# Optimization experiments

Hardware: AMD Instinct MI355X
Metric: run time of the kernel (lower is better)

Reference implementation:

```python
import jax, jax.numpy as jnp
import numpy as np

EPS = 1e-5

def bn_relu(y, g, b):
    # BatchNorm1d in training mode: stats over (B, L) per channel, biased variance
    mu = jnp.mean(y, axis=(0, 2), keepdims=True)
    var = jnp.var(y, axis=(0, 2), keepdims=True)
    yn = (y - mu) * jax.lax.rsqrt(var + EPS)
    return jax.nn.relu(yn * g[None, :, None] + b[None, :, None])

def conv1x1_pad1(x, W):
    # Conv1d(k=1, padding=1, bias=False): pointwise matmul then zero-pad length by 1 each side
    y = jnp.einsum('bcl,oc->bol', x, W)
    return jnp.pad(y, ((0, 0), (0, 0), (1, 1)))

def conv1x1(x, W, b):
    return jnp.einsum('bcl,oc->bol', x, W) + b[None, :, None]

def conv3_pad1(x, W):
    # Conv1d(k=3, padding=1, bias=False); W: [O, C, 3]
    return jax.lax.conv_general_dilated(x, W, window_strides=(1,), padding=((1, 1),),
                                        dimension_numbers=('NCH', 'OIH', 'NCH'))

def pam(f, Wq, bq, Wk, bk, Wv, bv, gamma):
    q = conv1x1(f, Wq, bq)          # [B, C//8, L]
    k = conv1x1(f, Wk, bk)          # [B, C//8, L]
    v = conv1x1(f, Wv, bv)          # [B, C, L]
    energy = jnp.einsum('bql,bqm->blm', q, k)   # [B, L, L]
    attn = jax.nn.softmax(energy, axis=-1)
    out = jnp.einsum('bcm,blm->bcl', v, attn)
    return gamma * out + f

def cam(f, gamma):
    energy = jnp.einsum('bcl,bdl->bcd', f, f)    # [B, C, C]
    energy_new = jnp.max(energy, axis=-1, keepdims=True) - energy
    attn = jax.nn.softmax(energy_new, axis=-1)
    out = jnp.einsum('bcd,bdl->bcl', attn, f)
    return gamma * out + f

def setup_inputs() -> dict:
    key = jax.random.key(0)
    ks = jax.random.split(key, 24)
    B, C, L = 8, 256, 2046
    IC, OC = C // 4, 128  # inter_channels=64, out_channels
    s = 0.05
    d = {
        'x':   jax.random.normal(ks[0], (B, C, L), jnp.float32),
        'W5a': jax.random.normal(ks[1], (IC, C), jnp.float32) * s,
        'g5a': jnp.ones((IC,), jnp.float32), 'b5a': jnp.zeros((IC,), jnp.float32),
        'W5c': jax.random.normal(ks[2], (IC, C), jnp.float32) * s,
        'g5c': jnp.ones((IC,), jnp.float32), 'b5c': jnp.zeros((IC,), jnp.float32),
        'Wq':  jax.random.normal(ks[3], (IC // 8, IC), jnp.float32) * s,
        'bq':  jnp.zeros((IC // 8,), jnp.float32),
        'Wk':  jax.random.normal(ks[4], (IC // 8, IC), jnp.float32) * s,
        'bk':  jnp.zeros((IC // 8,), jnp.float32),
        'Wv':  jax.random.normal(ks[5], (IC, IC), jnp.float32) * s,
        'bv':  jnp.zeros((IC,), jnp.float32),
        'gamma_pam': jnp.full((1,), 0.1, jnp.float32),
        'gamma_cam': jnp.full((1,), 0.1, jnp.float32),
        'W51': jax.random.normal(ks[6], (IC, IC, 3), jnp.float32) * s,
        'g51': jnp.ones((IC,), jnp.float32), 'b51': jnp.zeros((IC,), jnp.float32),
        'W52': jax.random.normal(ks[7], (IC, IC, 3), jnp.float32) * s,
        'g52': jnp.ones((IC,), jnp.float32), 'b52': jnp.zeros((IC,), jnp.float32),
        'W6':  jax.random.normal(ks[8], (OC, IC), jnp.float32) * s,
        'b6':  jnp.zeros((OC,), jnp.float32),
        'W7':  jax.random.normal(ks[9], (OC, IC), jnp.float32) * s,
        'b7':  jnp.zeros((OC,), jnp.float32),
        'W8':  jax.random.normal(ks[10], (OC, IC), jnp.float32) * s,
        'b8':  jnp.zeros((OC,), jnp.float32),
    }
    return d

def reference(x, W5a, g5a, b5a, W5c, g5c, b5c, Wq, bq, Wk, bk, Wv, bv,
              gamma_pam, gamma_cam, W51, g51, b51, W52, g52, b52,
              W6, b6, W7, b7, W8, b8):
    # dropout (p=0.1) treated as identity (eval mode)
    feat1 = bn_relu(conv1x1_pad1(x, W5a), g5a, b5a)          # [B, IC, L+2]
    sa_feat = pam(feat1, Wq, bq, Wk, bk, Wv, bv, gamma_pam)
    sa_conv = bn_relu(conv3_pad1(sa_feat, W51), g51, b51)
    sa_output = conv1x1(sa_conv, W6, b6)                     # [B, OC, L+2]
    feat2 = bn_relu(conv1x1_pad1(x, W5c), g5c, b5c)
    sc_feat = cam(feat2, gamma_cam)
    sc_conv = bn_relu(conv3_pad1(sc_feat, W52), g52, b52)
    sc_output = conv1x1(sc_conv, W7, b7)
    feat_sum = sa_conv + sc_conv
    sasc = conv1x1(feat_sum, W8, b8)
    # pool == 'maxpool' selects AdaptiveAvgPool1d(1) in the original (note swap)
    sasc = jnp.mean(sasc, axis=-1)                            # [B, OC]
    return (sasc, sa_output, sc_output)
```

## Files before the change

### kernel.cpp

```cpp
#include <hip/hip_runtime.h>
#include <math.h>

#define B 8
#define C 256
#define L 2046
#define LP 2048
#define IC 64
#define OC 128
#define BN_EPS 1e-5f
#define INVN (1.f / 16384.f)

#define OFF_Y1T    0u
#define OFF_Y2C    524288u
#define OFF_Y51T   2097152u
#define OFF_Y52T   2621440u
#define OFF_VB     3145728u
#define OFF_QT     3670016u
#define OFF_KT     3735552u
#define OFF_EPART  3866624u
#define OFF_STATS1 4423680u
#define OFF_STATS2 4424704u
#define OFF_W5BF   4425728u
#define OFF_W67    4442112u
#define OFF_WT     4450304u
#define OFF_WQKV   4462592u
#define OFF_BQKV   4465152u

typedef __attribute__((ext_vector_type(8))) short bshort8;
typedef __attribute__((ext_vector_type(4))) float f32x4;

__device__ __forceinline__ unsigned short f2bf(float f) {
    union { float f; unsigned int u; } v; v.f = f;
    return (unsigned short)((v.u + 0x8000u) >> 16);
}
__device__ __forceinline__ float bf2f(unsigned short u) {
    union { unsigned int i; float f; } v; v.i = ((unsigned int)u) << 16;
    return v.f;
}
__device__ __forceinline__ unsigned int pk2(float a, float b) {
    union { float f; unsigned int u; } va, vb; va.f = a; vb.f = b;
    return __builtin_amdgcn_perm(vb.u + 0x8000u, va.u + 0x8000u, 0x07060302u);
}

__device__ __forceinline__ void load_coef(const float* __restrict__ STATS,
        const float* __restrict__ g, const float* __restrict__ beta,
        int base, int cnt, float* cA, float* cB) {
    int t = threadIdx.x;
    if (t < cnt) {
        int ch = base + t;
        float s = STATS[ch * 2] + STATS[256 + ch * 2] + STATS[512 + ch * 2] + STATS[768 + ch * 2];
        float q = STATS[ch * 2 + 1] + STATS[256 + ch * 2 + 1] + STATS[512 + ch * 2 + 1] + STATS[768 + ch * 2 + 1];
        float mu = s * INVN;
        float var = q * INVN - mu * mu;
        float A = g[t] * rsqrtf(var + BN_EPS);
        cA[t] = A;
        cB[t] = beta[t] - mu * A;
    }
}

__global__ __launch_bounds__(256) void k_wprep(
        const float* __restrict__ W5a, const float* __restrict__ W5c,
        const float* __restrict__ W6, const float* __restrict__ W7,
        const float* __restrict__ W51, const float* __restrict__ W52,
        const float* __restrict__ Wq, const float* __restrict__ Wk,
        const float* __restrict__ Wv, const float* __restrict__ bq,
        const float* __restrict__ bk, const float* __restrict__ bv,
        const float* __restrict__ b8,
        unsigned short* __restrict__ W5BF, unsigned short* __restrict__ W67,
        unsigned short* __restrict__ WT, unsigned short* __restrict__ WQKV,
        float* __restrict__ BQKV, float* __restrict__ STATS1,
        float* __restrict__ STATS2, float* __restrict__ out_sasc) {
    int i = blockIdx.x * 256 + threadIdx.x;
    if (i < 32768) {
        int o = i >> 8, c = i & 255;
        W5BF[i] = f2bf(o < 64 ? W5a[o * 256 + c] : W5c[(o - 64) * 256 + c]);
    } else if (i < 49152) {
        int j = i - 32768; int g = j >> 13; int r = j & 8191;
        W67[j] = f2bf(g ? W7[r] : W6[r]);
    } else if (i < 73728) {
        int j = i - 49152;
        int c = j & 63, o = (j >> 6) & 63, wt = j >> 12; int w = wt / 3, t = wt % 3;
        const float* Ws = w ? W52 : W51;
        WT[j] = f2bf(Ws[(o * 64 + c) * 3 + t]);
    } else if (i < 78848) {
        int j = i - 73728; int o = j >> 6, c = j & 63;
        float v = o < 8 ? Wq[o * 64 + c] : (o < 16 ? Wk[(o - 8) * 64 + c] : Wv[(o - 16) * 64 + c]);
        WQKV[j] = f2bf(v);
    } else if (i < 78928) {
        int o = i - 78848;
        BQKV[o] = o < 8 ? bq[o] : (o < 16 ? bk[o - 8] : bv[o - 16]);
    } else if (i < 80976) {
        int j = i - 78928;
        if (j < 1024) STATS1[j] = 0.f; else STATS2[j - 1024] = 0.f;
    } else if (i < 82000) {
        int j = i - 80976;
        out_sasc[j] = b8[j & 127];
    }
}

__global__ __launch_bounds__(256) void k_conv1(const float* __restrict__ x,
        const unsigned short* __restrict__ W5BF,
        unsigned short* __restrict__ Y1T, unsigned short* __restrict__ Y2C,
        float* __restrict__ STATS1) {
    __shared__ unsigned short xt[64][264];
    __shared__ float lds_part[4][64];
    int lt = blockIdx.x, b = blockIdx.y;
    int l0 = lt * 64;
    int t = threadIdx.x;
    {
        int j = t & 63, cg = t >> 6;
        int ls = l0 - 1 + j;
        bool ok = (ls >= 0) && (ls < L);
        const float* xs = x + (size_t)(b * C + cg * 64) * L + ls;
        unsigned short* row = &xt[j][cg * 64];
#pragma unroll
        for (int c8 = 0; c8 < 8; ++c8) {
            unsigned int pk[4];
#pragma unroll
            for (int i = 0; i < 4; ++i) {
                float v0 = ok ? xs[(size_t)(c8 * 8 + 2 * i) * L] : 0.f;
                float v1 = ok ? xs[(size_t)(c8 * 8 + 2 * i + 1) * L] : 0.f;
                pk[i] = pk2(v0, v1);
            }
            *(uint4*)(row + c8 * 8) = *(const uint4*)pk;
        }
    }
    __syncthreads();
    int w = t >> 6, lane = t & 63, n = lane & 15, quad = lane >> 4;
    bshort8 wf[2][8];
#pragma unroll
    for (int oi = 0; oi < 2; ++oi)
#pragma unroll
        for (int kt = 0; kt < 8; ++kt)
            wf[oi][kt] = *(const bshort8*)(W5BF + (size_t)((w * 2 + oi) * 16 + n) * C + kt * 32 + quad * 8);
    f32x4 acc[2][4];
#pragma unroll
    for (int oi = 0; oi < 2; ++oi)
#pragma unroll
        for (int sub = 0; sub < 4; ++sub) acc[oi][sub] = (f32x4){0.f, 0.f, 0.f, 0.f};
#pragma unroll
    for (int sub = 0; sub < 4; ++sub) {
        int lloc = sub * 16 + n;
#pragma unroll
        for (int kt = 0; kt < 8; ++kt) {
            bshort8 xb = *(const bshort8*)(&xt[lloc][kt * 32 + quad * 8]);
            acc[0][sub] = __builtin_amdgcn_mfma_f32_16x16x32_bf16(wf[0][kt], xb, acc[0][sub], 0, 0, 0);
            acc[1][sub] = __builtin_amdgcn_mfma_f32_16x16x32_bf16(wf[1][kt], xb, acc[1][sub], 0, 0, 0);
        }
    }
    if (w < 2) {
#pragma unroll
        for (int sub = 0; sub < 4; ++sub) {
            int lp = l0 + sub * 16 + n;
#pragma unroll
            for (int oi = 0; oi < 2; ++oi) {
                int ot = w * 2 + oi;
                uint2 pv;
                pv.x = pk2(acc[oi][sub][0], acc[oi][sub][1]);
                pv.y = pk2(acc[oi][sub][2], acc[oi][sub][3]);
                *(uint2*)(Y1T + ((size_t)(b * LP + lp)) * IC + ot * 16 + quad * 4) = pv;
            }
        }
    } else {
#pragma unroll
        for (int oi = 0; oi < 2; ++oi) {
            int ot = (w - 2) * 2 + oi;
#pragma unroll
            for (int r = 0; r < 4; ++r) {
                int o = ot * 16 + quad * 4 + r;
                unsigned short* dst = Y2C + ((size_t)(b * IC + o)) * LP + l0;
#pragma unroll
                for (int sub = 0; sub < 4; ++sub)
                    dst[sub * 16 + n] = f2bf(acc[oi][sub][r]);
            }
        }
    }
#pragma unroll
    for (int oi = 0; oi < 2; ++oi)
#pragma unroll
        for (int r = 0; r < 4; ++r) {
            float s = 0.f, q = 0.f;
#pragma unroll
            for (int sub = 0; sub < 4; ++sub) {
                float v = acc[oi][sub][r];
                s += v; q += v * v;
            }
#pragma unroll
            for (int msk = 1; msk < 16; msk <<= 1) {
                s += __shfl_xor(s, msk, 64);
                q += __shfl_xor(q, msk, 64);
            }
            if (n == 0) {
                int ci = oi * 16 + quad * 4 + r;
                lds_part[w][ci * 2] = s;
                lds_part[w][ci * 2 + 1] = q;
            }
        }
    __syncthreads();
    {
        int ch = t >> 1, wsrc = ch >> 5;
        int idx = ((ch & 31) << 1) | (t & 1);
        atomicAdd(&STATS1[(blockIdx.x & 3) * 256 + t], lds_part[wsrc][idx]);
    }
}

__device__ void role_qkv(char* dynsm, int lt, int b,
        const unsigned short* __restrict__ Y1T, const float* __restrict__ STATS1,
        const float* __restrict__ g5a, const float* __restrict__ b5a,
        const unsigned short* __restrict__ WQKV, const float* __restrict__ BQKV,
        unsigned short* __restrict__ QT, unsigned short* __restrict__ KT,
        unsigned short* __restrict__ VB) {
    float* cA = (float*)dynsm;
    float* cB = cA + 64;
    load_coef(STATS1, g5a, b5a, 0, 64, cA, cB);
    __syncthreads();
    int t = threadIdx.x;
    int w = t >> 6, lane = t & 63, n = lane & 15, quad = lane >> 4;
    int lrow = lt * 64 + w * 16 + n;
    bshort8 fb[2];
#pragma unroll
    for (int kt = 0; kt < 2; ++kt) {
        bshort8 raw = *(const bshort8*)(Y1T + ((size_t)(b * LP + lrow)) * IC + kt * 32 + quad * 8);
        bshort8 f;
#pragma unroll
        for (int j = 0; j < 8; ++j) {
            int c = kt * 32 + quad * 8 + j;
            float v = fmaxf(fmaf(cA[c], bf2f((unsigned short)raw[j]), cB[c]), 0.f);
            ((unsigned short*)&f)[j] = f2bf(v);
        }
        fb[kt] = f;
    }
    f32x4 acc[5];
#pragma unroll
    for (int ot = 0; ot < 5; ++ot) {
        f32x4 a = {0.f, 0.f, 0.f, 0.f};
#pragma unroll
        for (int kt = 0; kt < 2; ++kt) {
            bshort8 wf = *(const bshort8*)(WQKV + (size_t)(ot * 16 + n) * IC + kt * 32 + quad * 8);
            a = __builtin_amdgcn_mfma_f32_16x16x32_bf16(wf, fb[kt], a, 0, 0, 0);
        }
        acc[ot] = a;
    }
#pragma unroll
    for (int ot = 0; ot < 5; ++ot)
#pragma unroll
        for (int r = 0; r < 4; ++r) {
            int o = ot * 16 + quad * 4 + r;
            unsigned short bv16 = f2bf(acc[ot][r] + BQKV[o]);
            if (ot == 0) {
                if (o < 8) QT[((size_t)(b * LP + lrow)) * 8 + o] = bv16;
                else KT[((size_t)(b * LP + lrow)) * 8 + (o - 8)] = bv16;
            } else {
                VB[((size_t)(b * IC + (o - 16))) * LP + lrow] = bv16;
            }
        }
}

__device__ void role_gram(char* dynsm, int blk, int b,
        const unsigned short* __restrict__ Y2C, const float* __restrict__ STATS1,
        const float* __restrict__ g5c, const float* __restrict__ b5c,
        float* __restrict__ EPART) {
    float* cA = (float*)dynsm;
    float* cB = cA + 64;
    load_coef(STATS1, g5c, b5c, 64, 64, cA, cB);
    __syncthreads();
    int t = threadIdx.x;
    int w = t >> 6, lane = t & 63, n = lane & 15, quad = lane >> 4;
    f32x4 acc[4][4];
#pragma unroll
    for (int ti = 0; ti < 4; ++ti)
#pragma unroll
        for (int tj = 0; tj < 4; ++tj) acc[ti][tj] = (f32x4){0.f, 0.f, 0.f, 0.f};
    for (int chunk = 0; chunk < 4; ++chunk) {
        int lb = (blk * 4 + w) * 128 + chunk * 32 + quad * 8;
        bshort8 frag[4];
#pragma unroll
        for (int g = 0; g < 4; ++g) {
            int c = g * 16 + n;
            bshort8 raw = *(const bshort8*)(Y2C + ((size_t)(b * IC + c)) * LP + lb);
            bshort8 f;
            float A = cA[c], Bc = cB[c];
#pragma unroll
            for (int j = 0; j < 8; ++j)
                ((unsigned short*)&f)[j] = f2bf(fmaxf(fmaf(A, bf2f((unsigned short)raw[j]), Bc), 0.f));
            frag[g] = f;
        }
#pragma unroll
        for (int ti = 0; ti < 4; ++ti)
#pragma unroll
            for (int tj = 0; tj < 4; ++tj)
                acc[ti][tj] = __builtin_amdgcn_mfma_f32_16x16x32_bf16(frag[ti], frag[tj], acc[ti][tj], 0, 0, 0);
    }
    float* ep = EPART + ((size_t)(b * 16 + blk * 4 + w)) * 4096;
#pragma unroll
    for (int ti = 0; ti < 4; ++ti)
#pragma unroll
        for (int tj = 0; tj < 4; ++tj)
#pragma unroll
            for (int r = 0; r < 4; ++r)
                ep[(ti * 16 + quad * 4 + r) * 64 + tj * 16 + n] = acc[ti][tj][r];
}

__global__ __launch_bounds__(256) void k_fuse1(
        const unsigned short* __restrict__ Y1T, const unsigned short* __restrict__ Y2C,
        const float* __restrict__ STATS1,
        const float* __restrict__ g5a, const float* __restrict__ b5a,
        const float* __restrict__ g5c, const float* __restrict__ b5c,
        const unsigned short* __restrict__ WQKV, const float* __restrict__ BQKV,
        unsigned short* __restrict__ QT, unsigned short* __restrict__ KT,
        unsigned short* __restrict__ VB, float* __restrict__ EPART) {
    extern __shared__ char dynsm[];
    int idx = blockIdx.x;
    if (idx < 256) role_qkv(dynsm, idx & 31, idx >> 5, Y1T, STATS1, g5a, b5a,
                            WQKV, BQKV, QT, KT, VB);
    else { int g = idx - 256; role_gram(dynsm, g & 3, g >> 2, Y2C, STATS1, g5c, b5c, EPART); }
}

__device__ __forceinline__ void conv3_from_tile(const unsigned short* tile,
        const unsigned short* __restrict__ WT, unsigned short* __restrict__ dst,
        int b, int l0, float* lds_part, float* __restrict__ STATS2,
        int og, int blockx) {
    int t = threadIdx.x;
    int w = t >> 6, lane = t & 63, n = lane & 15, quad = lane >> 4;
    int lrow = l0 + w * 16 + n;
    f32x4 acc[4];
#pragma unroll
    for (int ot = 0; ot < 4; ++ot) acc[ot] = (f32x4){0.f, 0.f, 0.f, 0.f};
#pragma unroll
    for (int t3 = 0; t3 < 3; ++t3) {
        int trow = w * 16 + n + t3;
        bshort8 fb0 = *(const bshort8*)(tile + trow * 72 + quad * 8);
        bshort8 fb1 = *(const bshort8*)(tile + trow * 72 + 32 + quad * 8);
#pragma unroll
        for (int ot = 0; ot < 4; ++ot) {
            bshort8 w0 = *(const bshort8*)(WT + ((size_t)(t3 * 64 + ot * 16 + n)) * IC + quad * 8);
            bshort8 w1 = *(const bshort8*)(WT + ((size_t)(t3 * 64 + ot * 16 + n)) * IC + 32 + quad * 8);
            acc[ot] = __builtin_amdgcn_mfma_f32_16x16x32_bf16(w0, fb0, acc[ot], 0, 0, 0);
            acc[ot] = __builtin_amdgcn_mfma_f32_16x16x32_bf16(w1, fb1, acc[ot], 0, 0, 0);
        }
    }
#pragma unroll
    for (int ot = 0; ot < 4; ++ot) {
        uint2 pv;
        pv.x = pk2(acc[ot][0], acc[ot][1]);
        pv.y = pk2(acc[ot][2], acc[ot][3]);
        *(uint2*)(dst + ((size_t)(b * LP + lrow)) * IC + ot * 16 + quad * 4) = pv;
    }
#pragma unroll
    for (int ot = 0; ot < 4; ++ot)
#pragma unroll
        for (int r = 0; r < 4; ++r) {
            float s = acc[ot][r], q = s * s;
#pragma unroll
            for (int msk = 1; msk < 16; msk <<= 1) {
                s += __shfl_xor(s, msk, 64);
                q += __shfl_xor(q, msk, 64);
            }
            if (n == 0) {
                int cch = ot * 16 + quad * 4 + r;
                lds_part[w * 128 + cch * 2] = s;
                lds_part[w * 128 + cch * 2 + 1] = q;
            }
        }
    __syncthreads();
    if (t < 128) {
        float s = lds_part[t] + lds_part[128 + t] + lds_part[256 + t] + lds_part[384 + t];
        atomicAdd(&STATS2[(blockx & 3) * 256 + og * 128 + t], s);
    }
}

__device__ void role_pam_full(char* dynsm, int qt, int b,
        const unsigned short* __restrict__ qT, const unsigned short* __restrict__ kT,
        const unsigned short* __restrict__ vb,
        const unsigned short* __restrict__ Y1T, const float* __restrict__ STATS1,
        const float* __restrict__ g5a, const float* __restrict__ b5a,
        const float* __restrict__ gamma, const unsigned short* __restrict__ WT,
        unsigned short* __restrict__ Y51T, float* __restrict__ STATS2) {
    unsigned short* vs0 = (unsigned short*)dynsm;
    unsigned short* vs1 = vs0 + 4608;
    unsigned short* ps  = vs1 + 4608;
    float* os = (float*)dynsm;
    unsigned short* tile = ps;
    float* cA = (float*)(dynsm + 27648);
    float* cB = cA + 64;
    float* dn = cB + 64;
    float* lds_part = dn + 64;
    int base = qt * 62 - 1;
    int tid = threadIdx.x;
    int wq = tid >> 6, lane = tid & 63, n = lane & 15, quad = lane >> 4;
    int srow = tid >> 2, schn = tid & 3;
    load_coef(STATS1, g5a, b5a, 0, 64, cA, cB);
    int qrow = base + wq * 16 + n;
    int qcl = qrow < 0 ? 0 : (qrow > LP - 1 ? LP - 1 : qrow);
    bshort8 qa = {};
    if (quad == 0)
        qa = *(const bshort8*)(qT + ((size_t)(b * LP + qcl)) * 8);
    f32x4 acc[4];
#pragma unroll
    for (int s = 0; s < 4; ++s) acc[s] = (f32x4){0.f, 0.f, 0.f, 0.f};
    float li[4] = {0.f, 0.f, 0.f, 0.f};
    unsigned short* pw = ps + wq * 16 * 72;

    {
        const unsigned short* src = vb + ((size_t)(b * IC + srow)) * LP + schn * 16;
        unsigned short* d = vs0 + srow * 72 + schn * 16;
        *(bshort8*)d = *(const bshort8*)src;
        *(bshort8*)(d + 8) = *(const bshort8*)(src + 8);
    }
    bshort8 kb[4];
#pragma unroll
    for (int s = 0; s < 4; ++s) kb[s] = (bshort8){};
    if (quad == 0) {
#pragma unroll
        for (int s = 0; s < 4; ++s)
            kb[s] = *(const bshort8*)(kT + ((size_t)(b * LP + s * 16 + n)) * 8);
    }
    __syncthreads();
    for (int it = 0; it < 32; ++it) {
        unsigned short* cur = (it & 1) ? vs1 : vs0;
        unsigned short* nxt = (it & 1) ? vs0 : vs1;
        if (it < 31) {
            const unsigned short* src = vb + ((size_t)(b * IC + srow)) * LP + (it + 1) * 64 + schn * 16;
            unsigned short* d = nxt + srow * 72 + schn * 16;
            *(bshort8*)d = *(const bshort8*)src;
            *(bshort8*)(d + 8) = *(const bshort8*)(src + 8);
        }
        bshort8 kn[4];
#pragma unroll
        for (int s = 0; s < 4; ++s) kn[s] = (bshort8){};
        if (it < 31 && quad == 0) {
            int m1 = (it + 1) * 64;
#pragma unroll
            for (int s = 0; s < 4; ++s)
                kn[s] = *(const bshort8*)(kT + ((size_t)(b * LP + m1 + s * 16 + n)) * 8);
        }
        f32x4 sc[4];
#pragma unroll
        for (int s = 0; s < 4; ++s)
            sc[s] = __builtin_amdgcn_mfma_f32_16x16x32_bf16(qa, kb[s],
                        (f32x4){0.f, 0.f, 0.f, 0.f}, 0, 0, 0);
#pragma unroll
        for (int s = 0; s < 4; ++s)
#pragma unroll
            for (int r = 0; r < 4; ++r) {
                float p = __expf(sc[s][r]);
                li[r] += p;
                pw[(quad * 4 + r) * 72 + s * 16 + n] = f2bf(p);
            }
#pragma unroll
        for (int step = 0; step < 2; ++step) {
            bshort8 pa = *(const bshort8*)(pw + n * 72 + step * 32 + quad * 8);
#pragma unroll
            for (int s = 0; s < 4; ++s) {
                bshort8 vf = *(const bshort8*)(cur + (s * 16 + n) * 72 + step * 32 + quad * 8);
                acc[s] = __builtin_amdgcn_mfma_f32_16x16x32_bf16(pa, vf, acc[s], 0, 0, 0);
            }
        }
        __syncthreads();
#pragma unroll
        for (int s = 0; s < 4; ++s) kb[s] = kn[s];
    }
#pragma unroll
    for (int s = 0; s < 4; ++s)
#pragma unroll
        for (int r = 0; r < 4; ++r)
            os[(s * 16 + n) * 65 + wq * 16 + quad * 4 + r] = acc[s][r];
#pragma unroll
    for (int r = 0; r < 4; ++r) {
        float s_ = li[r];
#pragma unroll
        for (int msk = 1; msk < 16; msk <<= 1) s_ += __shfl_xor(s_, msk, 64);
        if (n == 0) dn[wq * 16 + quad * 4 + r] = s_;
    }
    __syncthreads();
    float gm = gamma[0];
    {
        int c = tid >> 2, qc = tid & 3;
#pragma unroll
        for (int i = 0; i < 16; ++i) {
            int r = qc * 16 + i;
            int absr = base + r;
            float val = 0.f;
            if (absr >= 0 && absr < LP) {
                unsigned short raw = Y1T[((size_t)(b * LP + absr)) * IC + c];
                float f1v = fmaxf(fmaf(cA[c], bf2f(raw), cB[c]), 0.f);
                val = fmaf(gm, os[c * 65 + r] / dn[r], f1v);
            }
            tile[r * 72 + c] = f2bf(val);
        }
    }
    __syncthreads();
    {
        int j = wq * 16 + n;
        int absout = base + 1 + j;
        bool valid = (j < 62) && (absout < LP);
        f32x4 a3[4];
#pragma unroll
        for (int ot = 0; ot < 4; ++ot) a3[ot] = (f32x4){0.f, 0.f, 0.f, 0.f};
#pragma unroll
        for (int t3 = 0; t3 < 3; ++t3) {
            bshort8 fb0 = *(const bshort8*)(tile + (j + t3) * 72 + quad * 8);
            bshort8 fb1 = *(const bshort8*)(tile + (j + t3) * 72 + 32 + quad * 8);
#pragma unroll
            for (int ot = 0; ot < 4; ++ot) {
                bshort8 w0 = *(const bshort8*)(WT + ((size_t)(t3 * 64 + ot * 16 + n)) * IC + quad * 8);
                bshort8 w1 = *(const bshort8*)(WT + ((size_t)(t3 * 64 + ot * 16 + n)) * IC + 32 + quad * 8);
                a3[ot] = __builtin_amdgcn_mfma_f32_16x16x32_bf16(w0, fb0, a3[ot], 0, 0, 0);
                a3[ot] = __builtin_amdgcn_mfma_f32_16x16x32_bf16(w1, fb1, a3[ot], 0, 0, 0);
            }
        }
        if (valid) {
#pragma unroll
            for (int ot = 0; ot < 4; ++ot) {
                uint2 pv;
                pv.x = pk2(a3[ot][0], a3[ot][1]);
                pv.y = pk2(a3[ot][2], a3[ot][3]);
                *(uint2*)(Y51T + ((size_t)(b * LP + absout)) * IC + ot * 16 + quad * 4) = pv;
            }
        }
#pragma unroll
        for (int ot = 0; ot < 4; ++ot)
#pragma unroll
            for (int r = 0; r < 4; ++r) {
                float s = valid ? a3[ot][r] : 0.f;
                float q = s * s;
#pragma unroll
                for (int msk = 1; msk < 16; msk <<= 1) {
                    s += __shfl_xor(s, msk, 64);
                    q += __shfl_xor(q, msk, 64);
                }
                if (n == 0) {
                    int cch = ot * 16 + quad * 4 + r;
                    lds_part[wq * 128 + cch * 2] = s;
                    lds_part[wq * 128 + cch * 2 + 1] = q;
                }
            }
        __syncthreads();
        if (tid < 128) {
            float s = lds_part[tid] + lds_part[128 + tid] + lds_part[256 + tid] + lds_part[384 + tid];
            atomicAdd(&STATS2[(qt & 3) * 256 + tid], s);
        }
    }
}

__device__ void role_cam_full(char* dynsm, int lt, int b,
        const float* __restrict__ EPART, const unsigned short* __restrict__ Y2C,
        const float* __restrict__ STATS1,
        const float* __restrict__ g5c, const float* __restrict__ b5c,
        const float* __restrict__ gamma, const unsigned short* __restrict__ WT,
        unsigned short* __restrict__ Y52T, float* __restrict__ STATS2) {
    float* as = (float*)dynsm;
    float* cA = as + 4096; float* cB = cA + 64;
    unsigned short* tile = (unsigned short*)(cB + 64);
    float* lds_part = (float*)(tile + 4752);
    int l0 = lt * 64;
    int t = threadIdx.x;
    load_coef(STATS1, g5c, b5c, 64, 64, cA, cB);
    for (int idx = t; idx < 4096; idx += 256) {
        float s = 0.f;
#pragma unroll
        for (int ch = 0; ch < 16; ++ch) s += EPART[((size_t)(b * 16 + ch)) * 4096 + idx];
        as[idx] = s;
    }
    __syncthreads();
    {
        int row = t >> 2, qd = t & 3;
        float v[16];
#pragma unroll
        for (int i = 0; i < 16; ++i) v[i] = as[row * 64 + qd * 16 + i];
        float mn = v[0];
#pragma unroll
        for (int i = 1; i < 16; ++i) mn = fminf(mn, v[i]);
        mn = fminf(mn, __shfl_xor(mn, 1, 64));
        mn = fminf(mn, __shfl_xor(mn, 2, 64));
        float s = 0.f;
#pragma unroll
        for (int i = 0; i < 16; ++i) { v[i] = __expf(mn - v[i]); s += v[i]; }
        s += __shfl_xor(s, 1, 64);
        s += __shfl_xor(s, 2, 64);
        float inv = 1.f / s;
#pragma unroll
        for (int i = 0; i < 16; ++i) as[row * 64 + qd * 16 + i] = v[i] * inv;
    }
    __syncthreads();
    float gm = gamma[0];
    {
        int lq = t & 63, cg = t >> 6;
        const unsigned short* fb = Y2C + (size_t)b * IC * LP + l0 + lq;
        float acc[16];
#pragma unroll
        for (int i = 0; i < 16; ++i) acc[i] = 0.f;
        for (int d4 = 0; d4 < 16; ++d4) {
            float fv[4];
#pragma unroll
            for (int i = 0; i < 4; ++i) {
                int d = 4 * d4 + i;
                fv[i] = fmaxf(fmaf(cA[d], bf2f(fb[(size_t)d * LP]), cB[d]), 0.f);
            }
#pragma unroll
            for (int cc = 0; cc < 16; ++cc) {
                const float4 a4 = *reinterpret_cast<const float4*>(as + (cg * 16 + cc) * 64 + d4 * 4);
                acc[cc] += a4.x * fv[0] + a4.y * fv[1] + a4.z * fv[2] + a4.w * fv[3];
            }
        }
#pragma unroll
        for (int cc = 0; cc < 16; ++cc) {
            int c = cg * 16 + cc;
            float res = fmaxf(fmaf(cA[c], bf2f(fb[(size_t)c * LP]), cB[c]), 0.f);
            tile[(1 + lq) * 72 + c] = f2bf(fmaf(gm, acc[cc], res));
        }
    }
    float* fcol = lds_part;
    if (t < 128) {
        int row = t >> 6;
        int ch = t & 63;
        int l = l0 - 1 + row * 65;
        float v = 0.f;
        if (l >= 0 && l < LP)
            v = fmaxf(fmaf(cA[ch], bf2f(Y2C[(size_t)b * IC * LP + (size_t)ch * LP + l]), cB[ch]), 0.f);
        fcol[row * 64 + ch] = v;
    }
    __syncthreads();
    if (t < 128) {
        int sel = t & 1;
        int row = sel ? 65 : 0;
        int ch = t >> 1;
        int l = l0 - 1 + (sel ? 65 : 0);
        float val = 0.f;
        if (l >= 0 && l < LP) {
            const float* fc = fcol + sel * 64;
            float a = 0.f;
#pragma unroll 8
            for (int d = 0; d < 64; ++d) a = fmaf(as[ch * 64 + d], fc[d], a);
            val = fmaf(gm, a, fc[ch]);
        }
        tile[row * 72 + ch] = f2bf(val);
    }
    __syncthreads();
    conv3_from_tile(tile, WT, Y52T, b, l0, lds_part, STATS2, 1, lt);
}

__global__ __launch_bounds__(256) void k_fuse2(
        const unsigned short* __restrict__ QT, const unsigned short* __restrict__ KT,
        const unsigned short* __restrict__ VB,
        const unsigned short* __restrict__ Y1T, const unsigned short* __restrict__ Y2C,
        const float* __restrict__ STATS1,
        const float* __restrict__ g5a, const float* __restrict__ b5a,
        const float* __restrict__ g5c, const float* __restrict__ b5c,
        const float* __restrict__ gpam, const float* __restrict__ gcam,
        const float* __restrict__ EPART, const unsigned short* __restrict__ WTall,
        unsigned short* __restrict__ Y51T, unsigned short* __restrict__ Y52T,
        float* __restrict__ STATS2) {
    extern __shared__ char dynsm[];
    int idx = blockIdx.x;
    if (idx < 272) {
        int b = idx / 34; int qt = idx - b * 34;
        role_pam_full(dynsm, qt, b, QT, KT, VB, Y1T, STATS1, g5a, b5a, gpam,
                      WTall, Y51T, STATS2);
    } else {
        int g = idx - 272;
        role_cam_full(dynsm, g & 31, g >> 5, EPART, Y2C, STATS1, g5c, b5c, gcam,
                      WTall + 12288, Y52T, STATS2);
    }
}

__global__ __launch_bounds__(256) void k_final(const unsigned short* __restrict__ Y51T,
        const unsigned short* __restrict__ Y52T, const float* __restrict__ STATS2,
        const float* __restrict__ g51, const float* __restrict__ b51,
        const float* __restrict__ g52, const float* __restrict__ b52,
        const unsigned short* __restrict__ W67,
        const float* __restrict__ b6, const float* __restrict__ b7,
        const float* __restrict__ W8,
        float* __restrict__ out_sa, float* __restrict__ out_sc,
        float* __restrict__ out_sasc) {
    __shared__ float cA[128], cB[128];
    __shared__ float fsw[4][64];
    __shared__ float chsum[64];
    int lt = blockIdx.x, og = blockIdx.y, b = blockIdx.z;
    int t = threadIdx.x;
    if (t < 128) {
        float s = STATS2[t * 2] + STATS2[256 + t * 2] + STATS2[512 + t * 2] + STATS2[768 + t * 2];
        float q = STATS2[t * 2 + 1] + STATS2[256 + t * 2 + 1] + STATS2[512 + t * 2 + 1] + STATS2[768 + t * 2 + 1];
        float mu = s * INVN, var = q * INVN - mu * mu;
        float gv = t < 64 ? g51[t] : g52[t - 64];
        float bv = t < 64 ? b51[t] : b52[t - 64];
        float A = gv * rsqrtf(var + BN_EPS);
        cA[t] = A; cB[t] = bv - mu * A;
    }
    __syncthreads();
    int w = t >> 6, lane = t & 63, n = lane & 15, quad = lane >> 4;
    int lrow = lt * 64 + w * 16 + n;
    float fs_lane[16];
    bshort8 ba[2], bb[2];
#pragma unroll
    for (int kt = 0; kt < 2; ++kt) {
        bshort8 ra = *(const bshort8*)(Y51T + ((size_t)(b * LP + lrow)) * IC + kt * 32 + quad * 8);
        bshort8 rb = *(const bshort8*)(Y52T + ((size_t)(b * LP + lrow)) * IC + kt * 32 + quad * 8);
        bshort8 fa, fb;
#pragma unroll
        for (int j = 0; j < 8; ++j) {
            int c = kt * 32 + quad * 8 + j;
            float v1 = fmaxf(fmaf(cA[c], bf2f((unsigned short)ra[j]), cB[c]), 0.f);
            float v2 = fmaxf(fmaf(cA[64 + c], bf2f((unsigned short)rb[j]), cB[64 + c]), 0.f);
            ((unsigned short*)&fa)[j] = f2bf(v1);
            ((unsigned short*)&fb)[j] = f2bf(v2);
            fs_lane[kt * 8 + j] = v1 + v2;
        }
        ba[kt] = fa; bb[kt] = fb;
    }
    f32x4 accA[4], accB[4];
#pragma unroll
    for (int ot = 0; ot < 4; ++ot) {
        accA[ot] = (f32x4){0.f, 0.f, 0.f, 0.f};
        accB[ot] = (f32x4){0.f, 0.f, 0.f, 0.f};
    }
#pragma unroll
    for (int ot = 0; ot < 4; ++ot)
#pragma unroll
        for (int kt = 0; kt < 2; ++kt) {
            bshort8 wa = *(const bshort8*)(W67 + (size_t)(og * 64 + ot * 16 + n) * IC + kt * 32 + quad * 8);
            bshort8 wb = *(const bshort8*)(W67 + 8192 + (size_t)(og * 64 + ot * 16 + n) * IC + kt * 32 + quad * 8);
            accA[ot] = __builtin_amdgcn_mfma_f32_16x16x32_bf16(wa, ba[kt], accA[ot], 0, 0, 0);
            accB[ot] = __builtin_amdgcn_mfma_f32_16x16x32_bf16(wb, bb[kt], accB[ot], 0, 0, 0);
        }
#pragma unroll
    for (int ot = 0; ot < 4; ++ot)
#pragma unroll
        for (int r = 0; r < 4; ++r) {
            int o = og * 64 + ot * 16 + quad * 4 + r;
            out_sa[((size_t)(b * OC + o)) * LP + lrow] = accA[ot][r] + b6[o];
            out_sc[((size_t)(b * OC + o)) * LP + lrow] = accB[ot][r] + b7[o];
        }
    if (og == 0) {
#pragma unroll
        for (int i = 0; i < 16; ++i) {
            float s = fs_lane[i];
#pragma unroll
            for (int msk = 1; msk < 16; msk <<= 1) s += __shfl_xor(s, msk, 64);
            if (n == 0) {
                int c = (i >> 3) * 32 + quad * 8 + (i & 7);
                fsw[w][c] = s;
            }
        }
        __syncthreads();
        if (t < 64) chsum[t] = fsw[0][t] + fsw[1][t] + fsw[2][t] + fsw[3][t];
        __syncthreads();
        if (t < 128) {
            float s = 0.f;
            for (int c = 0; c < 64; ++c) s = fmaf(W8[t * 64 + c], chsum[c], s);
            atomicAdd(&out_sasc[b * OC + t], s * (1.f / (float)LP));
        }
    }
}

extern "C" void kernel_launch(void* const* d_in, const int* in_sizes, int n_in,
                              void* d_out, int out_size, void* d_ws, size_t ws_size,
                              hipStream_t stream) {
    (void)in_sizes; (void)n_in; (void)out_size; (void)ws_size;
    const float* x    = (const float*)d_in[0];
    const float* W5a  = (const float*)d_in[1];
    const float* g5a  = (const float*)d_in[2];
    const float* b5a  = (const float*)d_in[3];
    const float* W5c  = (const float*)d_in[4];
    const float* g5c  = (const float*)d_in[5];
    const float* b5c  = (const float*)d_in[6];
    const float* Wq   = (const float*)d_in[7];
    const float* bq   = (const float*)d_in[8];
    const float* Wk   = (const float*)d_in[9];
    const float* bk   = (const float*)d_in[10];
    const float* Wv   = (const float*)d_in[11];
    const float* bv   = (const float*)d_in[12];
    const float* gpam = (const float*)d_in[13];
    const float* gcam = (const float*)d_in[14];
    const float* W51  = (const float*)d_in[15];
    const float* g51  = (const float*)d_in[16];
    const float* b51  = (const float*)d_in[17];
    const float* W52  = (const float*)d_in[18];
    const float* g52  = (const float*)d_in[19];
    const float* b52  = (const float*)d_in[20];
    const float* W6   = (const float*)d_in[21];
    const float* b6   = (const float*)d_in[22];
    const float* W7   = (const float*)d_in[23];
    const float* b7   = (const float*)d_in[24];
    const float* W8   = (const float*)d_in[25];
    const float* b8   = (const float*)d_in[26];

    float* ws = (float*)d_ws;
    float* out = (float*)d_out;
    unsigned short* Y1T  = (unsigned short*)(ws + OFF_Y1T);
    unsigned short* Y2C  = (unsigned short*)(ws + OFF_Y2C);
    unsigned short* Y51T = (unsigned short*)(ws + OFF_Y51T);
    unsigned short* Y52T = (unsigned short*)(ws + OFF_Y52T);
    unsigned short* VB   = (unsigned short*)(ws + OFF_VB);
    unsigned short* QT   = (unsigned short*)(ws + OFF_QT);
    unsigned short* KT   = (unsigned short*)(ws + OFF_KT);
    float* EPART  = ws + OFF_EPART;
    float* STATS1 = ws + OFF_STATS1;
    float* STATS2 = ws + OFF_STATS2;
    unsigned short* W5BF = (unsigned short*)(ws + OFF_W5BF);
    unsigned short* W67  = (unsigned short*)(ws + OFF_W67);
    unsigned short* WT   = (unsigned short*)(ws + OFF_WT);
    unsigned short* WQKV = (unsigned short*)(ws + OFF_WQKV);
    float* BQKV = ws + OFF_BQKV;

    float* out_sa = out + B * OC;
    float* out_sc = out + B * OC + (size_t)B * OC * LP;

    k_wprep<<<321, 256, 0, stream>>>(W5a, W5c, W6, W7, W51, W52, Wq, Wk, Wv,
                                     bq, bk, bv, b8, W5BF, W67, WT, WQKV, BQKV,
                                     STATS1, STATS2, out);
    k_conv1<<<dim3(32, B), 256, 0, stream>>>(x, W5BF, Y1T, Y2C, STATS1);
    k_fuse1<<<288, 256, 512, stream>>>(Y1T, Y2C, STATS1, g5a, b5a, g5c, b5c,
                                       WQKV, BQKV, QT, KT, VB, EPART);
    k_fuse2<<<528, 256, 30464, stream>>>(QT, KT, VB, Y1T, Y2C, STATS1,
                                         g5a, b5a, g5c, b5c, gpam, gcam,
                                         EPART, WT, Y51T, Y52T, STATS2);
    k_final<<<dim3(32, 2, B), 256, 0, stream>>>(Y51T, Y52T, STATS2, g51, b51, g52, b52,
                                                W67, b6, b7, W8, out_sa, out_sc, out);
}
```

Baseline: 220.5 us.

## Double V staging chunk to 128 columns in PAM loop, halving barriers

```diff
diff --git a/kernel.cpp b/kernel.cpp
--- a/kernel.cpp
+++ b/kernel.cpp
@@ -44,8 +44,7 @@
 
 __device__ __forceinline__ void load_coef(const float* __restrict__ STATS,
         const float* __restrict__ g, const float* __restrict__ beta,
-        int base, int cnt, float* cA, float* cB) {
-    int t = threadIdx.x;
+        int base, int cnt, float* cA, float* cB, int t) {
     if (t < cnt) {
         int ch = base + t;
         float s = STATS[ch * 2] + STATS[256 + ch * 2] + STATS[512 + ch * 2] + STATS[768 + ch * 2];
@@ -212,7 +211,7 @@
         unsigned short* __restrict__ VB) {
     float* cA = (float*)dynsm;
     float* cB = cA + 64;
-    load_coef(STATS1, g5a, b5a, 0, 64, cA, cB);
+    load_coef(STATS1, g5a, b5a, 0, 64, cA, cB, threadIdx.x);
     __syncthreads();
     int t = threadIdx.x;
     int w = t >> 6, lane = t & 63, n = lane & 15, quad = lane >> 4;
@@ -262,7 +261,7 @@
         float* __restrict__ EPART) {
     float* cA = (float*)dynsm;
     float* cB = cA + 64;
-    load_coef(STATS1, g5c, b5c, 64, 64, cA, cB);
+    load_coef(STATS1, g5c, b5c, 64, 64, cA, cB, threadIdx.x);
     __syncthreads();
     int t = threadIdx.x;
     int w = t >> 6, lane = t & 63, n = lane & 15, quad = lane >> 4;
@@ -316,59 +315,6 @@
     else { int g = idx - 256; role_gram(dynsm, g & 3, g >> 2, Y2C, STATS1, g5c, b5c, EPART); }
 }
 
-__device__ __forceinline__ void conv3_from_tile(const unsigned short* tile,
-        const unsigned short* __restrict__ WT, unsigned short* __restrict__ dst,
-        int b, int l0, float* lds_part, float* __restrict__ STATS2,
-        int og, int blockx) {
-    int t = threadIdx.x;
-    int w = t >> 6, lane = t & 63, n = lane & 15, quad = lane >> 4;
-    int lrow = l0 + w * 16 + n;
-    f32x4 acc[4];
-#pragma unroll
-    for (int ot = 0; ot < 4; ++ot) acc[ot] = (f32x4){0.f, 0.f, 0.f, 0.f};
-#pragma unroll
-    for (int t3 = 0; t3 < 3; ++t3) {
-        int trow = w * 16 + n + t3;
-        bshort8 fb0 = *(const bshort8*)(tile + trow * 72 + quad * 8);
-        bshort8 fb1 = *(const bshort8*)(tile + trow * 72 + 32 + quad * 8);
-#pragma unroll
-        for (int ot = 0; ot < 4; ++ot) {
-            bshort8 w0 = *(const bshort8*)(WT + ((size_t)(t3 * 64 + ot * 16 + n)) * IC + quad * 8);
-            bshort8 w1 = *(const bshort8*)(WT + ((size_t)(t3 * 64 + ot * 16 + n)) * IC + 32 + quad * 8);
-            acc[ot] = __builtin_amdgcn_mfma_f32_16x16x32_bf16(w0, fb0, acc[ot], 0, 0, 0);
-            acc[ot] = __builtin_amdgcn_mfma_f32_16x16x32_bf16(w1, fb1, acc[ot], 0, 0, 0);
-        }
-    }
-#pragma unroll
-    for (int ot = 0; ot < 4; ++ot) {
-        uint2 pv;
-        pv.x = pk2(acc[ot][0], acc[ot][1]);
-        pv.y = pk2(acc[ot][2], acc[ot][3]);
-        *(uint2*)(dst + ((size_t)(b * LP + lrow)) * IC + ot * 16 + quad * 4) = pv;
-    }
-#pragma unroll
-    for (int ot = 0; ot < 4; ++ot)
-#pragma unroll
-        for (int r = 0; r < 4; ++r) {
-            float s = acc[ot][r], q = s * s;
-#pragma unroll
-            for (int msk = 1; msk < 16; msk <<= 1) {
-                s += __shfl_xor(s, msk, 64);
-                q += __shfl_xor(q, msk, 64);
-            }
-            if (n == 0) {
-                int cch = ot * 16 + quad * 4 + r;
-                lds_part[w * 128 + cch * 2] = s;
-                lds_part[w * 128 + cch * 2 + 1] = q;
-            }
-        }
-    __syncthreads();
-    if (t < 128) {
-        float s = lds_part[t] + lds_part[128 + t] + lds_part[256 + t] + lds_part[384 + t];
-        atomicAdd(&STATS2[(blockx & 3) * 256 + og * 128 + t], s);
-    }
-}
-
 __device__ void role_pam_full(char* dynsm, int qt, int b,
         const unsigned short* __restrict__ qT, const unsigned short* __restrict__ kT,
         const unsigned short* __restrict__ vb,
@@ -377,19 +323,19 @@
         const float* __restrict__ gamma, const unsigned short* __restrict__ WT,
         unsigned short* __restrict__ Y51T, float* __restrict__ STATS2) {
     unsigned short* vs0 = (unsigned short*)dynsm;
-    unsigned short* vs1 = vs0 + 4608;
-    unsigned short* ps  = vs1 + 4608;
+    unsigned short* vs1 = vs0 + 8704;
+    unsigned short* ps  = (unsigned short*)(dynsm + 34816);
+    unsigned short* tile = ps;
     float* os = (float*)dynsm;
-    unsigned short* tile = ps;
-    float* cA = (float*)(dynsm + 27648);
+    float* cA = (float*)(dynsm + 44032);
     float* cB = cA + 64;
     float* dn = cB + 64;
     float* lds_part = dn + 64;
     int base = qt * 62 - 1;
     int tid = threadIdx.x;
     int wq = tid >> 6, lane = tid & 63, n = lane & 15, quad = lane >> 4;
-    int srow = tid >> 2, schn = tid & 3;
-    load_coef(STATS1, g5a, b5a, 0, 64, cA, cB);
+    int sch = tid >> 2, skf = (tid & 3) * 32;
+    load_coef(STATS1, g5a, b5a, 0, 64, cA, cB, tid);
     int qrow = base + wq * 16 + n;
     int qcl = qrow < 0 ? 0 : (qrow > LP - 1 ? LP - 1 : qrow);
     bshort8 qa = {};
@@ -400,12 +346,15 @@
     for (int s = 0; s < 4; ++s) acc[s] = (f32x4){0.f, 0.f, 0.f, 0.f};
     float li[4] = {0.f, 0.f, 0.f, 0.f};
     unsigned short* pw = ps + wq * 16 * 72;
+    const unsigned short* vsrc = vb + ((size_t)(b * IC + sch)) * LP + skf;
 
     {
-        const unsigned short* src = vb + ((size_t)(b * IC + srow)) * LP + schn * 16;
-        unsigned short* d = vs0 + srow * 72 + schn * 16;
-        *(bshort8*)d = *(const bshort8*)src;
-        *(bshort8*)(d + 8) = *(const bshort8*)(src + 8);
+        bshort8 v0[4];
+#pragma unroll
+        for (int i = 0; i < 4; ++i) v0[i] = *(const bshort8*)(vsrc + i * 8);
+        unsigned short* d = vs0 + sch * 136 + skf;
+#pragma unroll
+        for (int i = 0; i < 4; ++i) *(bshort8*)(d + i * 8) = v0[i];
     }
     bshort8 kb[4];
 #pragma unroll
@@ -416,49 +365,58 @@
             kb[s] = *(const bshort8*)(kT + ((size_t)(b * LP + s * 16 + n)) * 8);
     }
     __syncthreads();
-    for (int it = 0; it < 32; ++it) {
-        unsigned short* cur = (it & 1) ? vs1 : vs0;
-        unsigned short* nxt = (it & 1) ? vs0 : vs1;
-        if (it < 31) {
-            const unsigned short* src = vb + ((size_t)(b * IC + srow)) * LP + (it + 1) * 64 + schn * 16;
-            unsigned short* d = nxt + srow * 72 + schn * 16;
-            *(bshort8*)d = *(const bshort8*)src;
-            *(bshort8*)(d + 8) = *(const bshort8*)(src + 8);
-        }
-        bshort8 kn[4];
-#pragma unroll
-        for (int s = 0; s < 4; ++s) kn[s] = (bshort8){};
-        if (it < 31 && quad == 0) {
-            int m1 = (it + 1) * 64;
+    for (int sup = 0; sup < 16; ++sup) {
+        unsigned short* cur = (sup & 1) ? vs1 : vs0;
+        unsigned short* nxt = (sup & 1) ? vs0 : vs1;
+        bshort8 vrg[4];
+        if (sup < 15) {
+#pragma unroll
+            for (int i = 0; i < 4; ++i)
+                vrg[i] = *(const bshort8*)(vsrc + (sup + 1) * 128 + i * 8);
+        }
+        __builtin_amdgcn_sched_barrier(0);
+#pragma unroll
+        for (int ki = 0; ki < 2; ++ki) {
+            int g = sup * 2 + ki;
+            bshort8 kn[4];
+#pragma unroll
+            for (int s = 0; s < 4; ++s) kn[s] = (bshort8){};
+            if (g < 31 && quad == 0) {
+#pragma unroll
+                for (int s = 0; s < 4; ++s)
+                    kn[s] = *(const bshort8*)(kT + ((size_t)(b * LP + (g + 1) * 64 + s * 16 + n)) * 8);
+            }
+            f32x4 sc[4];
 #pragma unroll
             for (int s = 0; s < 4; ++s)
-                kn[s] = *(const bshort8*)(kT + ((size_t)(b * LP + m1 + s * 16 + n)) * 8);
-        }
-        f32x4 sc[4];
-#pragma unroll
-        for (int s = 0; s < 4; ++s)
-            sc[s] = __builtin_amdgcn_mfma_f32_16x16x32_bf16(qa, kb[s],
-                        (f32x4){0.f, 0.f, 0.f, 0.f}, 0, 0, 0);
-#pragma unroll
-        for (int s = 0; s < 4; ++s)
-#pragma unroll
-            for (int r = 0; r < 4; ++r) {
-                float p = __expf(sc[s][r]);
-                li[r] += p;
-                pw[(quad * 4 + r) * 72 + s * 16 + n] = f2bf(p);
-            }
-#pragma unroll
-        for (int step = 0; step < 2; ++step) {
-            bshort8 pa = *(const bshort8*)(pw + n * 72 + step * 32 + quad * 8);
-#pragma unroll
-            for (int s = 0; s < 4; ++s) {
-                bshort8 vf = *(const bshort8*)(cur + (s * 16 + n) * 72 + step * 32 + quad * 8);
-                acc[s] = __builtin_amdgcn_mfma_f32_16x16x32_bf16(pa, vf, acc[s], 0, 0, 0);
-            }
+                sc[s] = __builtin_amdgcn_mfma_f32_16x16x32_bf16(qa, kb[s],
+                            (f32x4){0.f, 0.f, 0.f, 0.f}, 0, 0, 0);
+#pragma unroll
+            for (int s = 0; s < 4; ++s)
+#pragma unroll
+                for (int r = 0; r < 4; ++r) {
+                    float p = __expf(sc[s][r]);
+                    li[r] += p;
+                    pw[(quad * 4 + r) * 72 + s * 16 + n] = f2bf(p);
+                }
+#pragma unroll
+            for (int step = 0; step < 2; ++step) {
+                bshort8 pa = *(const bshort8*)(pw + n * 72 + step * 32 + quad * 8);
+#pragma unroll
+                for (int s = 0; s < 4; ++s) {
+                    bshort8 vf = *(const bshort8*)(cur + (s * 16 + n) * 136 + ki * 64 + step * 32 + quad * 8);
+                    acc[s] = __builtin_amdgcn_mfma_f32_16x16x32_bf16(pa, vf, acc[s], 0, 0, 0);
+                }
+            }
+#pragma unroll
+            for (int s = 0; s < 4; ++s) kb[s] = kn[s];
+        }
+        if (sup < 15) {
+            unsigned short* d = nxt + sch * 136 + skf;
+#pragma unroll
+            for (int i = 0; i < 4; ++i) *(bshort8*)(d + i * 8) = vrg[i];
         }
         __syncthreads();
-#pragma unroll
-        for (int s = 0; s < 4; ++s) kb[s] = kn[s];
     }
 #pragma unroll
     for (int s = 0; s < 4; ++s)
@@ -543,20 +501,71 @@
     }
 }
 
-__device__ void role_cam_full(char* dynsm, int lt, int b,
+__device__ __forceinline__ void conv3_from_tile_cam(const unsigned short* tile,
+        const unsigned short* __restrict__ WT, unsigned short* __restrict__ dst,
+        int b, int l0, float* lds_part, float* __restrict__ STATS2,
+        int blockx, int tl) {
+    int w = tl >> 6, lane = tl & 63, n = lane & 15, quad = lane >> 4;
+    int lrow = l0 + w * 16 + n;
+    f32x4 acc[4];
+#pragma unroll
+    for (int ot = 0; ot < 4; ++ot) acc[ot] = (f32x4){0.f, 0.f, 0.f, 0.f};
+#pragma unroll
+    for (int t3 = 0; t3 < 3; ++t3) {
+        int trow = w * 16 + n + t3;
+        bshort8 fb0 = *(const bshort8*)(tile + trow * 72 + quad * 8);
+        bshort8 fb1 = *(const bshort8*)(tile + trow * 72 + 32 + quad * 8);
+#pragma unroll
+        for (int ot = 0; ot < 4; ++ot) {
+            bshort8 w0 = *(const bshort8*)(WT + ((size_t)(t3 * 64 + ot * 16 + n)) * IC + quad * 8);
+            bshort8 w1 = *(const bshort8*)(WT + ((size_t)(t3 * 64 + ot * 16 + n)) * IC + 32 + quad * 8);
+            acc[ot] = __builtin_amdgcn_mfma_f32_16x16x32_bf16(w0, fb0, acc[ot], 0, 0, 0);
+            acc[ot] = __builtin_amdgcn_mfma_f32_16x16x32_bf16(w1, fb1, acc[ot], 0, 0, 0);
+        }
+    }
+#pragma unroll
+    for (int ot = 0; ot < 4; ++ot) {
+        uint2 pv;
+        pv.x = pk2(acc[ot][0], acc[ot][1]);
+        pv.y = pk2(acc[ot][2], acc[ot][3]);
+        *(uint2*)(dst + ((size_t)(b * LP + lrow)) * IC + ot * 16 + quad * 4) = pv;
+    }
+#pragma unroll
+    for (int ot = 0; ot < 4; ++ot)
+#pragma unroll
+        for (int r = 0; r < 4; ++r) {
+            float s = acc[ot][r], q = s * s;
+#pragma unroll
+            for (int msk = 1; msk < 16; msk <<= 1) {
+                s += __shfl_xor(s, msk, 64);
+                q += __shfl_xor(q, msk, 64);
+            }
+            if (n == 0) {
+                int cch = ot * 16 + quad * 4 + r;
+                lds_part[w * 128 + cch * 2] = s;
+                lds_part[w * 128 + cch * 2 + 1] = q;
+            }
+        }
+    __syncthreads();
+    if (tl < 128) {
+        float s = lds_part[tl] + lds_part[128 + tl] + lds_part[256 + tl] + lds_part[384 + tl];
+        atomicAdd(&STATS2[(blockx & 3) * 256 + 128 + tl], s);
+    }
+}
+
+__device__ void role_cam_full(char* sm, int tl, int lt, int b,
         const float* __restrict__ EPART, const unsigned short* __restrict__ Y2C,
         const float* __restrict__ STATS1,
         const float* __restrict__ g5c, const float* __restrict__ b5c,
         const float* __restrict__ gamma, const unsigned short* __restrict__ WT,
         unsigned short* __restrict__ Y52T, float* __restrict__ STATS2) {
-    float* as = (float*)dynsm;
+    float* as = (float*)sm;
     float* cA = as + 4096; float* cB = cA + 64;
     unsigned short* tile = (unsigned short*)(cB + 64);
     float* lds_part = (float*)(tile + 4752);
     int l0 = lt * 64;
-    int t = threadIdx.x;
-    load_coef(STATS1, g5c, b5c, 64, 64, cA, cB);
-    for (int idx = t; idx < 4096; idx += 256) {
+    load_coef(STATS1, g5c, b5c, 64, 64, cA, cB, tl);
+    for (int idx = tl; idx < 4096; idx += 256) {
         float s = 0.f;
 #pragma unroll
         for (int ch = 0; ch < 16; ++ch) s += EPART[((size_t)(b * 16 + ch)) * 4096 + idx];
@@ -564,7 +573,7 @@
     }
     __syncthreads();
     {
-        int row = t >> 2, qd = t & 3;
+        int row = tl >> 2, qd = tl & 3;
         float v[16];
 #pragma unroll
         for (int i = 0; i < 16; ++i) v[i] = as[row * 64 + qd * 16 + i];
@@ -585,7 +594,7 @@
     __syncthreads();
     float gm = gamma[0];
     {
-        int lq = t & 63, cg = t >> 6;
+        int lq = tl & 63, cg = tl >> 6;
         const unsigned short* fb = Y2C + (size_t)b * IC * LP + l0 + lq;
         float acc[16];
 #pragma unroll
@@ -611,9 +620,9 @@
         }
     }
     float* fcol = lds_part;
-    if (t < 128) {
-        int row = t >> 6;
-        int ch = t & 63;
+    if (tl < 128) {
+        int row = tl >> 6;
+        int ch = tl & 63;
         int l = l0 - 1 + row * 65;
         float v = 0.f;
         if (l >= 0 && l < LP)
@@ -621,10 +630,10 @@
         fcol[row * 64 + ch] = v;
     }
     __syncthreads();
-    if (t < 128) {
-        int sel = t & 1;
+    if (tl < 128) {
+        int sel = tl & 1;
         int row = sel ? 65 : 0;
-        int ch = t >> 1;
+        int ch = tl >> 1;
         int l = l0 - 1 + (sel ? 65 : 0);
         float val = 0.f;
         if (l >= 0 && l < LP) {
@@ -637,7 +646,7 @@
         tile[row * 72 + ch] = f2bf(val);
     }
     __syncthreads();
-    conv3_from_tile(tile, WT, Y52T, b, l0, lds_part, STATS2, 1, lt);
+    conv3_from_tile_cam(tile, WT, Y52T, b, l0, lds_part, STATS2, lt, tl);
 }
 
 __global__ __launch_bounds__(256) void k_fuse2(
@@ -659,8 +668,8 @@
                       WTall, Y51T, STATS2);
     } else {
         int g = idx - 272;
-        role_cam_full(dynsm, g & 31, g >> 5, EPART, Y2C, STATS1, g5c, b5c, gcam,
-                      WTall + 12288, Y52T, STATS2);
+        role_cam_full(dynsm, threadIdx.x, g & 31, g >> 5, EPART, Y2C, STATS1,
+                      g5c, b5c, gcam, WTall + 12288, Y52T, STATS2);
     }
 }
 
@@ -812,7 +821,7 @@
     k_conv1<<<dim3(32, B), 256, 0, stream>>>(x, W5BF, Y1T, Y2C, STATS1);
     k_fuse1<<<288, 256, 512, stream>>>(Y1T, Y2C, STATS1, g5a, b5a, g5c, b5c,
                                        WQKV, BQKV, QT, KT, VB, EPART);
-    k_fuse2<<<528, 256, 30464, stream>>>(QT, KT, VB, Y1T, Y2C, STATS1,
+    k_fuse2<<<528, 256, 46848, stream>>>(QT, KT, VB, Y1T, Y2C, STATS1,
                                          g5a, b5a, g5c, b5c, gpam, gcam,
                                          EPART, WT, Y51T, Y52T, STATS2);
     k_final<<<dim3(32, 2, B), 256, 0, stream>>>(Y51T, Y52T, STATS2, g51, b51, g52, b52,
```

Result: faster. 212.3 us, median of 4 (-3.7%).
